# Optimization experiments

Measured on AMD Instinct MI355X. Metric: run time of the kernel, lower is better.

## Reference

```python
import jax, jax.numpy as jnp
import numpy as np
from jax import lax

B, C, H, W = 4, 64, 128, 128
G, K, RED = 16, 7, 4        # groups, kernel size, reduce ratio
CR = C // RED               # reduced channels for kernel generation
EPS = 1e-5                  # BatchNorm eps (torch default)
DN = ('NCHW', 'OIHW', 'NCHW')


def setup_inputs() -> dict:
    key = jax.random.key(0)
    ks = jax.random.split(key, 5)
    return {
        'input': jax.random.normal(ks[0], (B, C, H, W), jnp.float32),
        # initial_mapping: depthwise 3x3 conv + pointwise 1x1 conv (bias=False)
        'w_dw': jax.random.normal(ks[1], (C, 1, 3, 3), jnp.float32) * 0.1,
        'w_pw': jax.random.normal(ks[2], (C, C), jnp.float32) * (1.0 / np.sqrt(C)),
        # sigma_mapping BatchNorm affine params
        'bn_gamma': jnp.ones((CR,), jnp.float32),
        'bn_beta': jnp.zeros((CR,), jnp.float32),
        # reduce / span 1x1 convs (bias=False)
        'w_reduce': jax.random.normal(ks[3], (CR, C), jnp.float32) * (1.0 / np.sqrt(C)),
        'w_span': jax.random.normal(ks[4], (K * K * G, CR), jnp.float32) * (1.0 / np.sqrt(CR)),
    }


def reference(input, w_dw, w_pw, bn_gamma, bn_beta, w_reduce, w_span):
    x = input
    # initial mapping: depthwise 3x3 (pad 1) then 1x1 pointwise
    h = lax.conv_general_dilated(x, w_dw, (1, 1), [(1, 1), (1, 1)],
                                 feature_group_count=C, dimension_numbers=DN)
    h = jnp.einsum('bchw,oc->bohw', h, w_pw)
    # unfold -> [B, C*K*K, H, W] with channel-major feature ordering (matches torch Unfold)
    patches = lax.conv_general_dilated_patches(h, (K, K), (1, 1), [(3, 3), (3, 3)],
                                               dimension_numbers=DN)
    patches = patches.reshape(B, G, C // G, K * K, H, W)
    # kernel generation: o_mapping is identity (stride 1 avg pool), then reduce -> BN(train) -> ReLU -> span
    r = jnp.einsum('bchw,oc->bohw', x, w_reduce)           # [B, CR, H, W]
    mean = r.mean(axis=(0, 2, 3), keepdims=True)
    var = r.var(axis=(0, 2, 3), keepdims=True)             # biased var, as torch BN training
    r = (r - mean) * lax.rsqrt(var + EPS) * bn_gamma[None, :, None, None] + bn_beta[None, :, None, None]
    r = jax.nn.relu(r)
    kern = jnp.einsum('bchw,oc->bohw', r, w_span)          # [B, G*K*K, H, W]
    kern = kern.reshape(B, G, 1, K * K, H, W)
    out = (kern * patches).sum(axis=3)                     # [B, G, C//G, H, W]
    return out.reshape(B, C, H, W)
```

## Files before the change

### kernel.cpp

```cpp
#include <hip/hip_runtime.h>

typedef _Float16 half2v __attribute__((ext_vector_type(2)));
typedef _Float16 half4v __attribute__((ext_vector_type(4)));
typedef _Float16 half8v __attribute__((ext_vector_type(8)));
typedef float f32x4 __attribute__((ext_vector_type(4)));

__launch_bounds__(256, 4)
__global__ void k_front(const float* __restrict__ in, const float* __restrict__ wdw,
                        const float* __restrict__ wpw, const float* __restrict__ wred,
                        _Float16* __restrict__ h16, _Float16* __restrict__ r16,
                        float* __restrict__ partial){
  __shared__ float4 s_in4[4][10][12];
  __shared__ __attribute__((aligned(16))) _Float16 s_dwh[64][72];
  __shared__ __attribute__((aligned(16))) _Float16 s_cvh[64][72];
  __shared__ float s_red[4][32];
  int t = threadIdx.x;
  int w = t >> 6, lane = t & 63;
  int lx = lane & 7, ly = lane >> 3;
  int c15 = lane & 15, hi = lane >> 4;
  int blk0 = blockIdx.x;

  int blk = ((blk0 & 7) << 7) | (blk0 >> 3);
  int tile = blk & 255, b = blk >> 8;
  int x0 = (tile & 15) << 3, y0 = (tile >> 4) << 3;
  const float* inb = in + ((long)b << 20) + ((long)(w << 2) << 14);

  const float* ap = wpw + (((w << 4) + c15) << 6) + (hi << 3);
  float4 ap0 = *(const float4*)(ap);
  float4 ap1 = *(const float4*)(ap + 4);
  float4 ap2 = *(const float4*)(ap + 32);
  float4 ap3 = *(const float4*)(ap + 36);
  const float* arp = wred + (c15 << 6) + (hi << 3);
  float4 ar0 = *(const float4*)(arp);
  float4 ar1 = *(const float4*)(arp + 4);
  float4 ar2 = *(const float4*)(arp + 32);
  float4 ar3 = *(const float4*)(arp + 36);
  half8v a_pw0 = {(_Float16)ap0.x,(_Float16)ap0.y,(_Float16)ap0.z,(_Float16)ap0.w,
                  (_Float16)ap1.x,(_Float16)ap1.y,(_Float16)ap1.z,(_Float16)ap1.w};
  half8v a_pw1 = {(_Float16)ap2.x,(_Float16)ap2.y,(_Float16)ap2.z,(_Float16)ap2.w,
                  (_Float16)ap3.x,(_Float16)ap3.y,(_Float16)ap3.z,(_Float16)ap3.w};
  half8v a_rd0 = {(_Float16)ar0.x,(_Float16)ar0.y,(_Float16)ar0.z,(_Float16)ar0.w,
                  (_Float16)ar1.x,(_Float16)ar1.y,(_Float16)ar1.z,(_Float16)ar1.w};
  half8v a_rd1 = {(_Float16)ar2.x,(_Float16)ar2.y,(_Float16)ar2.z,(_Float16)ar2.w,
                  (_Float16)ar3.x,(_Float16)ar3.y,(_Float16)ar3.z,(_Float16)ar3.w};

  int p1 = lane + 64;
  int ry0 = lane / 10, rx0 = lane - ry0 * 10;
  int ry1 = p1 / 10,   rx1 = p1 - ry1 * 10;
  int yy0 = y0 + ry0 - 1, xx0 = x0 + rx0 - 1;
  int yy1 = y0 + ry1 - 1, xx1 = x0 + rx1 - 1;
  bool ok0 = (unsigned)yy0 < 128u && (unsigned)xx0 < 128u;
  bool ok1 = (p1 < 100) && ((unsigned)yy1 < 128u) && ((unsigned)xx1 < 128u);
  int o0 = (yy0 << 7) + xx0, o1 = (yy1 << 7) + xx1;

  auto dw_dep = [&](int q){
    int wdbase = __builtin_amdgcn_readfirstlane(((q << 4) + (w << 2)) * 9);
    const float* wd = wdw + wdbase;
    float4 a = make_float4(0.f,0.f,0.f,0.f);
    float4 cv = make_float4(0.f,0.f,0.f,0.f);
    #pragma unroll
    for (int dy = 0; dy < 3; dy++){
      #pragma unroll
      for (int dx = 0; dx < 3; dx++){
        float4 v = s_in4[w][ly + dy][lx + dx];
        int k = dy * 3 + dx;
        a.x += v.x * wd[k];
        a.y += v.y * wd[9 + k];
        a.z += v.z * wd[18 + k];
        a.w += v.w * wd[27 + k];
        if (k == 4) cv = v;
      }
    }
    int cb = (q << 4) + (w << 2);
    half4v ah = {(_Float16)a.x,(_Float16)a.y,(_Float16)a.z,(_Float16)a.w};
    half4v eh = {(_Float16)cv.x,(_Float16)cv.y,(_Float16)cv.z,(_Float16)cv.w};
    *(half4v*)&s_dwh[lane][cb] = ah;
    *(half4v*)&s_cvh[lane][cb] = eh;
  };

  float4 vA0 = make_float4(0.f,0.f,0.f,0.f), vA1 = vA0, vB0 = vA0, vB1 = vA0;
  if (ok0){ vA0.x = inb[o0]; vA0.y = inb[o0+16384]; vA0.z = inb[o0+32768]; vA0.w = inb[o0+49152]; }
  if (ok1){ vA1.x = inb[o1]; vA1.y = inb[o1+16384]; vA1.z = inb[o1+32768]; vA1.w = inb[o1+49152]; }
  {
    const float* p1q = inb + (1L << 18);
    if (ok0){ vB0.x = p1q[o0]; vB0.y = p1q[o0+16384]; vB0.z = p1q[o0+32768]; vB0.w = p1q[o0+49152]; }
    if (ok1){ vB1.x = p1q[o1]; vB1.y = p1q[o1+16384]; vB1.z = p1q[o1+32768]; vB1.w = p1q[o1+49152]; }
  }

  #pragma unroll
  for (int qq = 0; qq < 2; qq++){
    s_in4[w][ry0][rx0] = vA0;
    if (p1 < 100) s_in4[w][ry1][rx1] = vA1;
    __builtin_amdgcn_wave_barrier();
    if (qq == 0){
      const float* pq = inb + (2L << 18);
      vA0 = make_float4(0.f,0.f,0.f,0.f); vA1 = vA0;
      if (ok0){ vA0.x = pq[o0]; vA0.y = pq[o0+16384]; vA0.z = pq[o0+32768]; vA0.w = pq[o0+49152]; }
      if (ok1){ vA1.x = pq[o1]; vA1.y = pq[o1+16384]; vA1.z = pq[o1+32768]; vA1.w = pq[o1+49152]; }
    }
    dw_dep(qq << 1);
    __builtin_amdgcn_wave_barrier();

    s_in4[w][ry0][rx0] = vB0;
    if (p1 < 100) s_in4[w][ry1][rx1] = vB1;
    __builtin_amdgcn_wave_barrier();
    if (qq == 0){
      const float* pq = inb + (3L << 18);
      vB0 = make_float4(0.f,0.f,0.f,0.f); vB1 = vB0;
      if (ok0){ vB0.x = pq[o0]; vB0.y = pq[o0+16384]; vB0.z = pq[o0+32768]; vB0.w = pq[o0+49152]; }
      if (ok1){ vB1.x = pq[o1]; vB1.y = pq[o1+16384]; vB1.z = pq[o1+32768]; vB1.w = pq[o1+49152]; }
    }
    dw_dep((qq << 1) + 1);
    __builtin_amdgcn_wave_barrier();
  }

  __syncthreads();

  f32x4 z = {0.f,0.f,0.f,0.f};
  f32x4 acc[4] = {z, z, z, z};
  #pragma unroll
  for (int tt = 0; tt < 4; tt++){
    half8v b0 = *(const half8v*)&s_dwh[(tt << 4) + c15][hi << 3];
    half8v b1 = *(const half8v*)&s_dwh[(tt << 4) + c15][32 + (hi << 3)];
    acc[tt] = __builtin_amdgcn_mfma_f32_16x16x32_f16(a_pw0, b0, acc[tt], 0, 0, 0);
    acc[tt] = __builtin_amdgcn_mfma_f32_16x16x32_f16(a_pw1, b1, acc[tt], 0, 0, 0);
  }
  #pragma unroll
  for (int tt = 0; tt < 4; tt++){
    int px = (tt << 4) + c15;
    int pyl = px >> 3, pxl = px & 7;
    int gout = (w << 2) + hi;
    long off = ((((long)((b << 4) + gout)) << 14) + ((y0 + pyl) << 7) + x0 + pxl) << 2;
    half4v hv = {(_Float16)acc[tt][0], (_Float16)acc[tt][1],
                 (_Float16)acc[tt][2], (_Float16)acc[tt][3]};
    *(half4v*)&h16[off] = hv;
  }

  f32x4 rac = z;
  {
    half8v b0 = *(const half8v*)&s_cvh[(w << 4) + c15][hi << 3];
    half8v b1 = *(const half8v*)&s_cvh[(w << 4) + c15][32 + (hi << 3)];
    rac = __builtin_amdgcn_mfma_f32_16x16x32_f16(a_rd0, b0, rac, 0, 0, 0);
    rac = __builtin_amdgcn_mfma_f32_16x16x32_f16(a_rd1, b1, rac, 0, 0, 0);
  }
  {
    int px = (w << 4) + c15;
    int pyl = px >> 3, pxl = px & 7;
    long roff = ((((long)b << 14) + ((y0 + pyl) << 7) + x0 + pxl) << 4) + (hi << 2);
    half4v rv4 = {(_Float16)rac[0], (_Float16)rac[1], (_Float16)rac[2], (_Float16)rac[3]};
    *(half4v*)&r16[roff] = rv4;
  }

  #pragma unroll
  for (int rr = 0; rr < 4; rr++){
    float v = rac[rr], s2 = v * v;
    #pragma unroll
    for (int m = 1; m < 16; m <<= 1){
      v  += __shfl_xor(v,  m, 64);
      s2 += __shfl_xor(s2, m, 64);
    }
    if (c15 == 0){
      int ch = (hi << 2) + rr;
      s_red[w][2 * ch]     = v;
      s_red[w][2 * ch + 1] = s2;
    }
  }
  __syncthreads();
  if (t < 32)
    partial[(blk0 << 5) + t] = s_red[0][t] + s_red[1][t] + s_red[2][t] + s_red[3][t];
}

__global__ void k_red(const float* __restrict__ partial, const float* __restrict__ gamma,
                      const float* __restrict__ beta, float* __restrict__ sb,
                      const float* __restrict__ wspan, _Float16* __restrict__ w16){
  __shared__ float sp[1024];
  int t = threadIdx.x;
  int c = t & 31, grp = t >> 5;
  float s = 0.f;
  #pragma unroll 4
  for (int i = grp; i < 1024; i += 32) s += partial[(i << 5) + c];
  sp[t] = s;
  for (int i = t; i < 12544; i += 1024) w16[i] = (_Float16)wspan[i];
  __syncthreads();
  if (t < 32){
    float v = 0.f;
    #pragma unroll
    for (int k = 0; k < 32; k++) v += sp[(k << 5) + t];
    sp[t] = v;
  }
  __syncthreads();
  if (t < 16){
    const float inv_n = 1.52587890625e-5f;
    float mean = sp[2 * t] * inv_n;
    float var  = sp[2 * t + 1] * inv_n - mean * mean;
    float inv  = rsqrtf(var + 1e-5f);
    float sc   = gamma[t] * inv;
    sb[2 * t]     = sc;
    sb[2 * t + 1] = beta[t] - mean * sc;
  }
}

__launch_bounds__(256)
__global__ void k_main(const _Float16* __restrict__ h16, const _Float16* __restrict__ r16,
                       const float* __restrict__ sb, const _Float16* __restrict__ w16,
                       float* __restrict__ out){
  __shared__ float4 s_h4[22][38];
  __shared__ float  s_sb[32];
  int t = threadIdx.x;
  int g = blockIdx.y, b = blockIdx.z;
  int bx = blockIdx.x;
  bx = ((bx & 7) << 2) | (bx >> 3);
  int tx0 = (bx & 3) << 5, ty0 = (bx >> 2) << 4;
  int ltx = t & 15, lty = t >> 4;
  int pxA = tx0 + (ltx << 1), py = ty0 + lty;

  const _Float16* rp = r16 + ((((long)b << 14) + (py << 7) + pxA) << 4);
  half8v raA = *(const half8v*)rp;
  half8v rbA = *(const half8v*)(rp + 8);
  half8v raB = *(const half8v*)(rp + 16);
  half8v rbB = *(const half8v*)(rp + 24);

  const _Float16* hp = h16 + (((long)((b << 4) + g)) << 16);
  for (int p = t; p < 836; p += 256){
    int ry = p / 38, rx = p - ry * 38;
    int yy = ty0 + ry - 3, xx = tx0 + rx - 3;
    float4 v = make_float4(0.f,0.f,0.f,0.f);
    if ((unsigned)yy < 128u && (unsigned)xx < 128u){
      half4v hh = *(const half4v*)&hp[(long)(((yy << 7) + xx) << 2)];
      v = make_float4((float)hh[0], (float)hh[1], (float)hh[2], (float)hh[3]);
    }
    s_h4[ry][rx] = v;
  }
  if (t < 32) s_sb[t] = sb[t];
  __syncthreads();

  half2v rvA[8], rvB[8];
  {
    float rv[16];
    #pragma unroll
    for (int c = 0; c < 8; c++){
      rv[c]     = fmaxf((float)raA[c] * s_sb[2*c]     + s_sb[2*c+1],     0.f);
      rv[c + 8] = fmaxf((float)rbA[c] * s_sb[2*(c+8)] + s_sb[2*(c+8)+1], 0.f);
    }
    #pragma unroll
    for (int j = 0; j < 8; j++){
      half2v pk; pk[0] = (_Float16)rv[2*j]; pk[1] = (_Float16)rv[2*j+1];
      rvA[j] = pk;
    }
    #pragma unroll
    for (int c = 0; c < 8; c++){
      rv[c]     = fmaxf((float)raB[c] * s_sb[2*c]     + s_sb[2*c+1],     0.f);
      rv[c + 8] = fmaxf((float)rbB[c] * s_sb[2*(c+8)] + s_sb[2*(c+8)+1], 0.f);
    }
    #pragma unroll
    for (int j = 0; j < 8; j++){
      half2v pk; pk[0] = (_Float16)rv[2*j]; pk[1] = (_Float16)rv[2*j+1];
      rvB[j] = pk;
    }
  }

  const _Float16* wg = w16 + g * 784;
  const half2v* wg2 = (const half2v*)wg;

  float aA0 = 0.f, aA1 = 0.f, aA2 = 0.f, aA3 = 0.f;
  float aB0 = 0.f, aB1 = 0.f, aB2 = 0.f, aB3 = 0.f;

  #pragma unroll 1
  for (int kh = 0; kh < 7; kh++){
    float4 row[8];
    #pragma unroll
    for (int j = 0; j < 8; j++) row[j] = s_h4[lty + kh][(ltx << 1) + j];
    #pragma unroll
    for (int kw = 0; kw < 7; kw++){
      int k = kh * 7 + kw;
      float kvA0 = 0.f, kvA1 = 0.f, kvB0 = 0.f, kvB1 = 0.f;
#if __has_builtin(__builtin_amdgcn_fdot2)
      #pragma unroll
      for (int j = 0; j < 4; j++){
        half2v w0 = wg2[k*8 + j], w1 = wg2[k*8 + j + 4];
        kvA0 = __builtin_amdgcn_fdot2(rvA[j],     w0, kvA0, false);
        kvA1 = __builtin_amdgcn_fdot2(rvA[j + 4], w1, kvA1, false);
        kvB0 = __builtin_amdgcn_fdot2(rvB[j],     w0, kvB0, false);
        kvB1 = __builtin_amdgcn_fdot2(rvB[j + 4], w1, kvB1, false);
      }
#else
      #pragma unroll
      for (int j = 0; j < 4; j++){
        half2v w0 = wg2[k*8 + j], w1 = wg2[k*8 + j + 4];
        kvA0 += (float)rvA[j][0]*(float)w0[0]   + (float)rvA[j][1]*(float)w0[1];
        kvA1 += (float)rvA[j+4][0]*(float)w1[0] + (float)rvA[j+4][1]*(float)w1[1];
        kvB0 += (float)rvB[j][0]*(float)w0[0]   + (float)rvB[j][1]*(float)w0[1];
        kvB1 += (float)rvB[j+4][0]*(float)w1[0] + (float)rvB[j+4][1]*(float)w1[1];
      }
#endif
      float kvA = kvA0 + kvA1, kvB = kvB0 + kvB1;
      float4 hA = row[kw], hB = row[kw + 1];
      aA0 += kvA * hA.x;  aB0 += kvB * hB.x;
      aA1 += kvA * hA.y;  aB1 += kvB * hB.y;
      aA2 += kvA * hA.z;  aB2 += kvB * hB.z;
      aA3 += kvA * hA.w;  aB3 += kvB * hB.w;
    }
  }

  long obase = (((long)((b << 6) + (g << 2))) << 14) + (py << 7) + pxA;
  *(float2*)&out[obase]         = make_float2(aA0, aB0);
  *(float2*)&out[obase + 16384] = make_float2(aA1, aB1);
  *(float2*)&out[obase + 32768] = make_float2(aA2, aB2);
  *(float2*)&out[obase + 49152] = make_float2(aA3, aB3);
}

extern "C" void kernel_launch(void* const* d_in, const int* in_sizes, int n_in,
                              void* d_out, int out_size, void* d_ws, size_t ws_size,
                              hipStream_t stream){
  const float* in       = (const float*)d_in[0];
  const float* w_dw     = (const float*)d_in[1];
  const float* w_pw     = (const float*)d_in[2];
  const float* gamma    = (const float*)d_in[3];
  const float* beta     = (const float*)d_in[4];
  const float* w_reduce = (const float*)d_in[5];
  const float* w_span   = (const float*)d_in[6];
  float* out = (float*)d_out;

  _Float16* h16 = (_Float16*)d_ws;
  _Float16* r16 = h16 + 4194304;
  _Float16* w16 = r16 + 1048576;
  float* partial = (float*)(w16 + 16384);
  float* sb      = partial + 32768;

  k_front<<<1024, 256, 0, stream>>>(in, w_dw, w_pw, w_reduce, h16, r16, partial);
  k_red  <<<1, 1024, 0, stream>>>(partial, gamma, beta, sb, w_span, w16);
  dim3 grid(32, 16, 4);
  k_main <<<grid, 256, 0, stream>>>(h16, r16, sb, w16, out);
}
```

Measured before the change: 125.0 us.

## Shrink k_main to single-wave 16x8 tiles and prefetch all front inputs upfront

k_main now runs 64-thread blocks over 16x8 pixel tiles instead of 256-thread blocks over 32x16 tiles. This quadruples the grid, replaces __syncthreads with a wave barrier, and reads the BN scale/bias straight from global memory instead of staging it in shared memory. Smaller tiles carry a larger halo relative to the tile, so more h16 data is reloaded per output pixel. k_front issues all four channel-quad input loads up front instead of double-buffering them, which raises register pressure in exchange for more loads in flight.

```diff
diff --git a/kernel.cpp b/kernel.cpp
--- a/kernel.cpp
+++ b/kernel.cpp
@@ -24,6 +24,25 @@
   int tile = blk & 255, b = blk >> 8;
   int x0 = (tile & 15) << 3, y0 = (tile >> 4) << 3;
   const float* inb = in + ((long)b << 20) + ((long)(w << 2) << 14);
+
+  int p1 = lane + 64;
+  int ry0 = lane / 10, rx0 = lane - ry0 * 10;
+  int ry1 = p1 / 10,   rx1 = p1 - ry1 * 10;
+  int yy0 = y0 + ry0 - 1, xx0 = x0 + rx0 - 1;
+  int yy1 = y0 + ry1 - 1, xx1 = x0 + rx1 - 1;
+  bool ok0 = (unsigned)yy0 < 128u && (unsigned)xx0 < 128u;
+  bool ok1 = (p1 < 100) && ((unsigned)yy1 < 128u) && ((unsigned)xx1 < 128u);
+  int o0 = (yy0 << 7) + xx0, o1 = (yy1 << 7) + xx1;
+
+  float4 vb0[4], vb1[4];
+  #pragma unroll
+  for (int q = 0; q < 4; q++){
+    const float* pq = inb + ((long)q << 18);
+    float4 a = make_float4(0.f,0.f,0.f,0.f), bb = a;
+    if (ok0){ a.x  = pq[o0]; a.y  = pq[o0+16384]; a.z  = pq[o0+32768]; a.w  = pq[o0+49152]; }
+    if (ok1){ bb.x = pq[o1]; bb.y = pq[o1+16384]; bb.z = pq[o1+32768]; bb.w = pq[o1+49152]; }
+    vb0[q] = a; vb1[q] = bb;
+  }
 
   const float* ap = wpw + (((w << 4) + c15) << 6) + (hi << 3);
   float4 ap0 = *(const float4*)(ap);
@@ -44,16 +63,12 @@
   half8v a_rd1 = {(_Float16)ar2.x,(_Float16)ar2.y,(_Float16)ar2.z,(_Float16)ar2.w,
                   (_Float16)ar3.x,(_Float16)ar3.y,(_Float16)ar3.z,(_Float16)ar3.w};
 
-  int p1 = lane + 64;
-  int ry0 = lane / 10, rx0 = lane - ry0 * 10;
-  int ry1 = p1 / 10,   rx1 = p1 - ry1 * 10;
-  int yy0 = y0 + ry0 - 1, xx0 = x0 + rx0 - 1;
-  int yy1 = y0 + ry1 - 1, xx1 = x0 + rx1 - 1;
-  bool ok0 = (unsigned)yy0 < 128u && (unsigned)xx0 < 128u;
-  bool ok1 = (p1 < 100) && ((unsigned)yy1 < 128u) && ((unsigned)xx1 < 128u);
-  int o0 = (yy0 << 7) + xx0, o1 = (yy1 << 7) + xx1;
-
-  auto dw_dep = [&](int q){
+  #pragma unroll
+  for (int q = 0; q < 4; q++){
+    s_in4[w][ry0][rx0] = vb0[q];
+    if (p1 < 100) s_in4[w][ry1][rx1] = vb1[q];
+    __builtin_amdgcn_wave_barrier();
+
     int wdbase = __builtin_amdgcn_readfirstlane(((q << 4) + (w << 2)) * 9);
     const float* wd = wdw + wdbase;
     float4 a = make_float4(0.f,0.f,0.f,0.f);
@@ -76,41 +91,6 @@
     half4v eh = {(_Float16)cv.x,(_Float16)cv.y,(_Float16)cv.z,(_Float16)cv.w};
     *(half4v*)&s_dwh[lane][cb] = ah;
     *(half4v*)&s_cvh[lane][cb] = eh;
-  };
-
-  float4 vA0 = make_float4(0.f,0.f,0.f,0.f), vA1 = vA0, vB0 = vA0, vB1 = vA0;
-  if (ok0){ vA0.x = inb[o0]; vA0.y = inb[o0+16384]; vA0.z = inb[o0+32768]; vA0.w = inb[o0+49152]; }
-  if (ok1){ vA1.x = inb[o1]; vA1.y = inb[o1+16384]; vA1.z = inb[o1+32768]; vA1.w = inb[o1+49152]; }
-  {
-    const float* p1q = inb + (1L << 18);
-    if (ok0){ vB0.x = p1q[o0]; vB0.y = p1q[o0+16384]; vB0.z = p1q[o0+32768]; vB0.w = p1q[o0+49152]; }
-    if (ok1){ vB1.x = p1q[o1]; vB1.y = p1q[o1+16384]; vB1.z = p1q[o1+32768]; vB1.w = p1q[o1+49152]; }
-  }
-
-  #pragma unroll
-  for (int qq = 0; qq < 2; qq++){
-    s_in4[w][ry0][rx0] = vA0;
-    if (p1 < 100) s_in4[w][ry1][rx1] = vA1;
-    __builtin_amdgcn_wave_barrier();
-    if (qq == 0){
-      const float* pq = inb + (2L << 18);
-      vA0 = make_float4(0.f,0.f,0.f,0.f); vA1 = vA0;
-      if (ok0){ vA0.x = pq[o0]; vA0.y = pq[o0+16384]; vA0.z = pq[o0+32768]; vA0.w = pq[o0+49152]; }
-      if (ok1){ vA1.x = pq[o1]; vA1.y = pq[o1+16384]; vA1.z = pq[o1+32768]; vA1.w = pq[o1+49152]; }
-    }
-    dw_dep(qq << 1);
-    __builtin_amdgcn_wave_barrier();
-
-    s_in4[w][ry0][rx0] = vB0;
-    if (p1 < 100) s_in4[w][ry1][rx1] = vB1;
-    __builtin_amdgcn_wave_barrier();
-    if (qq == 0){
-      const float* pq = inb + (3L << 18);
-      vB0 = make_float4(0.f,0.f,0.f,0.f); vB1 = vB0;
-      if (ok0){ vB0.x = pq[o0]; vB0.y = pq[o0+16384]; vB0.z = pq[o0+32768]; vB0.w = pq[o0+49152]; }
-      if (ok1){ vB1.x = pq[o1]; vB1.y = pq[o1+16384]; vB1.z = pq[o1+32768]; vB1.w = pq[o1+49152]; }
-    }
-    dw_dep((qq << 1) + 1);
     __builtin_amdgcn_wave_barrier();
   }
 
@@ -200,18 +180,17 @@
   }
 }
 
-__launch_bounds__(256)
+__launch_bounds__(64, 3)
 __global__ void k_main(const _Float16* __restrict__ h16, const _Float16* __restrict__ r16,
                        const float* __restrict__ sb, const _Float16* __restrict__ w16,
                        float* __restrict__ out){
-  __shared__ float4 s_h4[22][38];
-  __shared__ float  s_sb[32];
-  int t = threadIdx.x;
+  __shared__ float4 s_h4[14][23];
+  int lane = threadIdx.x;
   int g = blockIdx.y, b = blockIdx.z;
   int bx = blockIdx.x;
-  bx = ((bx & 7) << 2) | (bx >> 3);
-  int tx0 = (bx & 3) << 5, ty0 = (bx >> 2) << 4;
-  int ltx = t & 15, lty = t >> 4;
+  bx = ((bx & 7) << 4) | (bx >> 3);
+  int tx0 = (bx & 7) << 4, ty0 = (bx >> 3) << 3;
+  int ltx = lane & 7, lty = lane >> 3;
   int pxA = tx0 + (ltx << 1), py = ty0 + lty;
 
   const _Float16* rp = r16 + ((((long)b << 14) + (py << 7) + pxA) << 4);
@@ -221,26 +200,29 @@
   half8v rbB = *(const half8v*)(rp + 24);
 
   const _Float16* hp = h16 + (((long)((b << 4) + g)) << 16);
-  for (int p = t; p < 836; p += 256){
-    int ry = p / 38, rx = p - ry * 38;
-    int yy = ty0 + ry - 3, xx = tx0 + rx - 3;
-    float4 v = make_float4(0.f,0.f,0.f,0.f);
-    if ((unsigned)yy < 128u && (unsigned)xx < 128u){
-      half4v hh = *(const half4v*)&hp[(long)(((yy << 7) + xx) << 2)];
-      v = make_float4((float)hh[0], (float)hh[1], (float)hh[2], (float)hh[3]);
-    }
-    s_h4[ry][rx] = v;
-  }
-  if (t < 32) s_sb[t] = sb[t];
-  __syncthreads();
+  #pragma unroll
+  for (int i = 0; i < 5; i++){
+    int p = lane + (i << 6);
+    if (p < 308){
+      int ry = p / 22, rx = p - ry * 22;
+      int yy = ty0 + ry - 3, xx = tx0 + rx - 3;
+      float4 v = make_float4(0.f,0.f,0.f,0.f);
+      if ((unsigned)yy < 128u && (unsigned)xx < 128u){
+        half4v hh = *(const half4v*)&hp[(long)(((yy << 7) + xx) << 2)];
+        v = make_float4((float)hh[0], (float)hh[1], (float)hh[2], (float)hh[3]);
+      }
+      s_h4[ry][rx] = v;
+    }
+  }
+  __builtin_amdgcn_wave_barrier();
 
   half2v rvA[8], rvB[8];
   {
     float rv[16];
     #pragma unroll
     for (int c = 0; c < 8; c++){
-      rv[c]     = fmaxf((float)raA[c] * s_sb[2*c]     + s_sb[2*c+1],     0.f);
-      rv[c + 8] = fmaxf((float)rbA[c] * s_sb[2*(c+8)] + s_sb[2*(c+8)+1], 0.f);
+      rv[c]     = fmaxf((float)raA[c] * sb[2*c]     + sb[2*c+1],     0.f);
+      rv[c + 8] = fmaxf((float)rbA[c] * sb[2*(c+8)] + sb[2*(c+8)+1], 0.f);
     }
     #pragma unroll
     for (int j = 0; j < 8; j++){
@@ -249,8 +231,8 @@
     }
     #pragma unroll
     for (int c = 0; c < 8; c++){
-      rv[c]     = fmaxf((float)raB[c] * s_sb[2*c]     + s_sb[2*c+1],     0.f);
-      rv[c + 8] = fmaxf((float)rbB[c] * s_sb[2*(c+8)] + s_sb[2*(c+8)+1], 0.f);
+      rv[c]     = fmaxf((float)raB[c] * sb[2*c]     + sb[2*c+1],     0.f);
+      rv[c + 8] = fmaxf((float)rbB[c] * sb[2*(c+8)] + sb[2*(c+8)+1], 0.f);
     }
     #pragma unroll
     for (int j = 0; j < 8; j++){
@@ -329,6 +311,6 @@
 
   k_front<<<1024, 256, 0, stream>>>(in, w_dw, w_pw, w_reduce, h16, r16, partial);
   k_red  <<<1, 1024, 0, stream>>>(partial, gamma, beta, sb, w_span, w16);
-  dim3 grid(32, 16, 4);
-  k_main <<<grid, 256, 0, stream>>>(h16, r16, sb, w16, out);
+  dim3 grid(128, 16, 4);
+  k_main <<<grid, 64, 0, stream>>>(h16, r16, sb, w16, out);
 }
```

After: 128.4 us. 1.03x slower.
